# Optimization experiments

Measured on AMD Instinct MI355X. Metric: run time of the kernel, lower is better.

## Reference

```python
import jax, jax.numpy as jnp
import numpy as np

B, S, D, H = 2, 2048, 64, 12  # batch, seq, richness (per-head dim), heads
NEG = -99999.0


def setup_inputs() -> dict:
    key = jax.random.key(0)
    ks = jax.random.split(key, 9)
    s_in = 1.0 / np.sqrt(D)
    s_out = 1.0 / np.sqrt(H * D)
    return {
        "x": jax.random.normal(ks[0], (B, S, D), dtype=jnp.float32),
        "Wq": jax.random.uniform(ks[1], (D, H * D), jnp.float32, -s_in, s_in),
        "bq": jax.random.uniform(ks[2], (H * D,), jnp.float32, -s_in, s_in),
        "Wk": jax.random.uniform(ks[3], (D, H * D), jnp.float32, -s_in, s_in),
        "bk": jax.random.uniform(ks[4], (H * D,), jnp.float32, -s_in, s_in),
        "Wv": jax.random.uniform(ks[5], (D, H * D), jnp.float32, -s_in, s_in),
        "bv": jax.random.uniform(ks[6], (H * D,), jnp.float32, -s_in, s_in),
        "Wo": jax.random.uniform(ks[7], (H * D, D), jnp.float32, -s_out, s_out),
        "bo": jax.random.uniform(ks[8], (D,), jnp.float32, -s_out, s_out),
    }


def reference(x, Wq, bq, Wk, bk, Wv, bv, Wo, bo):
    b, s, d = x.shape
    def split_heads(y):
        return y.reshape(b, s, H, d).transpose(0, 2, 1, 3)  # [B,H,S,D]
    q = split_heads(x @ Wq + bq)
    k = split_heads(x @ Wk + bk)
    v = split_heads(x @ Wv + bv)
    # NOTE: no 1/sqrt(d) scaling, faithful to original module.
    scores = jnp.einsum("bhqd,bhkd->bhqk", q, k)  # [B,H,S,S]
    # Faithful quirky mask: tril of the scores, then mask where it's zero.
    mask = jnp.tril(scores)
    scores = jnp.where(mask == 0, NEG, scores)
    p = jax.nn.softmax(scores, axis=-1)
    o = jnp.einsum("bhqk,bhkd->bhqd", p, v)  # [B,H,S,D]
    o = o.transpose(0, 2, 1, 3).reshape(b, s, H * d)
    return o @ Wo + bo
```

## Files before the change

### kernel.cpp

```cpp
#include <hip/hip_runtime.h>
#include <math.h>
#include <type_traits>

#define BB 2
#define SS 2048
#define DD 64
#define HH 12
#define C2FIX 23.083120654223414f

typedef _Float16 v8h __attribute__((ext_vector_type(8)));
typedef short    v8s __attribute__((ext_vector_type(8)));
typedef short    v4s __attribute__((ext_vector_type(4)));
typedef float    v4f __attribute__((ext_vector_type(4)));
typedef unsigned int v2u __attribute__((ext_vector_type(2)));

__device__ __forceinline__ unsigned short f2bf(float f) {
    unsigned u = __float_as_uint(f);
    u += 0x7FFF + ((u >> 16) & 1);
    return (unsigned short)(u >> 16);
}

__device__ __forceinline__ void async16(const void* g, void* l) {
    __builtin_amdgcn_global_load_lds(
        (const __attribute__((address_space(1))) unsigned int*)g,
        (__attribute__((address_space(3))) unsigned int*)l, 16, 0, 0);
}

__global__ __launch_bounds__(256) void prep_kernel(
    const float* __restrict__ x,
    const float* __restrict__ Wq, const float* __restrict__ Wk,
    const float* __restrict__ Wv, const float* __restrict__ Wo,
    _Float16* __restrict__ x16, _Float16* __restrict__ W16,
    _Float16* __restrict__ WoT)
{
    const int idx = blockIdx.x * 256 + threadIdx.x;
    if (idx < 262144) {
        x16[idx] = (_Float16)x[idx];
    } else if (idx < 262144 + 147456) {
        const int t = idx - 262144;
        const int k = t / 2304, c = t % 2304;
        const int mat = c / 768, cc = c % 768;
        const float* W = (mat == 0) ? Wq : (mat == 1) ? Wk : Wv;
        W16[c * 64 + k] = (_Float16)W[k * 768 + cc];
    } else {
        const int e = idx - 262144 - 147456;
        WoT[(e & 63) * 768 + (e >> 6)] = (_Float16)Wo[e];
    }
}

__global__ __launch_bounds__(256) void qkv_kernel(
    const _Float16* __restrict__ x16, const _Float16* __restrict__ W16,
    const float* __restrict__ bq, const float* __restrict__ bk,
    const float* __restrict__ bv,
    _Float16* __restrict__ Q16, _Float16* __restrict__ K16,
    unsigned short* __restrict__ VT)
{
    const int r0  = blockIdx.x * 64;
    const int c0g = blockIdx.y * 64;
    const int mat = c0g / 768, cc0 = c0g % 768;
    const int h   = cc0 >> 6;
    const int b   = r0 >> 11, s0 = r0 & 2047;

    const int wave = threadIdx.x >> 6, lane = threadIdx.x & 63;
    const int llow = lane & 15, quad = lane >> 4;
    const int rowbase = r0 + 16 * wave;

    const float* bias = (mat == 0) ? bq : (mat == 1) ? bk : bv;

    v8h a0 = *(const v8h*)(x16 + (size_t)(rowbase + llow) * 64 + quad * 8);
    v8h a1 = *(const v8h*)(x16 + (size_t)(rowbase + llow) * 64 + 32 + quad * 8);

    v4f acc[4];
    float bv4[4];
#pragma unroll
    for (int nb = 0; nb < 4; nb++) {
        const int col = c0g + 16 * nb + llow;
        v8h b0 = *(const v8h*)(W16 + (size_t)col * 64 + quad * 8);
        v8h b1 = *(const v8h*)(W16 + (size_t)col * 64 + 32 + quad * 8);
        v4f a = (v4f){0.f, 0.f, 0.f, 0.f};
        a = __builtin_amdgcn_mfma_f32_16x16x32_f16(a0, b0, a, 0, 0, 0);
        a = __builtin_amdgcn_mfma_f32_16x16x32_f16(a1, b1, a, 0, 0, 0);
        acc[nb] = a;
        bv4[nb] = bias[cc0 + 16 * nb + llow];
    }

    const int bh = b * HH + h;
    if (mat == 0) {
#pragma unroll
        for (int nb = 0; nb < 4; nb++)
#pragma unroll
            for (int r = 0; r < 4; r++) {
                const int s = s0 + 16 * wave + quad * 4 + r;
                Q16[((size_t)bh * SS + s) * 64 + 16 * nb + llow] =
                    (_Float16)((acc[nb][r] + bv4[nb]) * 1.4426950408889634f);
            }
    } else if (mat == 1) {
#pragma unroll
        for (int nb = 0; nb < 4; nb++)
#pragma unroll
            for (int r = 0; r < 4; r++) {
                const int s = s0 + 16 * wave + quad * 4 + r;
                K16[((size_t)bh * SS + s) * 64 + 16 * nb + llow] =
                    (_Float16)(acc[nb][r] + bv4[nb]);
            }
    } else {
#pragma unroll
        for (int nb = 0; nb < 4; nb++) {
            const int d = 16 * nb + llow;
            const int s = s0 + 16 * wave + quad * 4;
            unsigned short p0 = f2bf(acc[nb][0] + bv4[nb]);
            unsigned short p1 = f2bf(acc[nb][1] + bv4[nb]);
            unsigned short p2 = f2bf(acc[nb][2] + bv4[nb]);
            unsigned short p3 = f2bf(acc[nb][3] + bv4[nb]);
            v2u pk = (v2u){(unsigned)p0 | ((unsigned)p1 << 16),
                           (unsigned)p2 | ((unsigned)p3 << 16)};
            *(v2u*)&VT[((size_t)bh * 64 + d) * SS + s] = pk;
        }
    }
}

__global__ __launch_bounds__(256, 3) void attn_kernel(
    const _Float16* __restrict__ Q16, const _Float16* __restrict__ K16,
    const unsigned short* __restrict__ VTg, _Float16* __restrict__ O16)
{
    __shared__ __align__(16) _Float16       Kl[3][64 * 64];
    __shared__ __align__(16) unsigned short Vl[3][64 * 64];

    const int bh    = blockIdx.y;
    const int qtile = (int)((blockIdx.x + 11 * blockIdx.y) & 31);
    const int qBase = qtile * 64;
    const int wave  = threadIdx.x >> 6;
    const int lane  = threadIdx.x & 63;
    const int llow  = lane & 15;
    const int quad  = lane >> 4;
    const int q0    = qBase + 16 * wave;

    const _Float16*       Kp = K16 + (size_t)bh * SS * 64;
    const unsigned short* Vp = VTg + (size_t)bh * 64 * SS;

    const _Float16* Qp = Q16 + ((size_t)bh * SS + q0) * 64;
    v8h qa0 = *(const v8h*)(Qp + llow * 64 + quad * 8);
    v8h qa1 = *(const v8h*)(Qp + llow * 64 + 32 + quad * 8);

    v4f o[4];
    v4f ls = (v4f){0.f, 0.f, 0.f, 0.f};
    const short one_bf = (short)0x3F80;
    const v4s vones = (v4s){one_bf, one_bf, one_bf, one_bf};
#pragma unroll
    for (int nb = 0; nb < 4; nb++) o[nb] = (v4f){0.f, 0.f, 0.f, 0.f};

    const int nt = qtile + 1;
    const int qrow = q0 + llow;
    const int sw = llow & 7;

    auto stage = [&](int kt, int b) {
#pragma unroll
        for (int rep = 0; rep < 2; rep++) {
            int c = rep * 256 + threadIdx.x;
            int row = c >> 3, g = (c & 7) ^ (row & 7);
            async16(Kp + (size_t)(kt + row) * 64 + g * 8,
                    &Kl[b][(rep * 256 + wave * 64) * 8]);
            async16(Vp + (size_t)row * SS + kt + g * 8,
                    &Vl[b][(rep * 256 + wave * 64) * 8]);
        }
    };

    stage(0, 0);
    if (nt > 1) stage(64, 1);

    auto round_body = [&](int t, auto masked_c) {
        constexpr bool MASKED = decltype(masked_c)::value;
        if constexpr (MASKED)
            asm volatile("s_waitcnt vmcnt(0)" ::: "memory");
        else
            asm volatile("s_waitcnt vmcnt(4)" ::: "memory");
        __builtin_amdgcn_s_barrier();
        __builtin_amdgcn_sched_barrier(0);
        if (t + 2 < nt) stage((t + 2) * 64, (t + 2) % 3);
        const int buf = t % 3, kt = t * 64;

        v4f sc[4];
#pragma unroll
        for (int cb = 0; cb < 4; cb++) {
            const int rk = 16 * cb + llow;
            v8h k0 = *(const v8h*)&Kl[buf][rk * 64 + ((quad ^ sw)) * 8];
            v8h k1 = *(const v8h*)&Kl[buf][rk * 64 + (((4 + quad) ^ sw)) * 8];
            v4f a2 = (v4f){0.f, 0.f, 0.f, 0.f};
            a2 = __builtin_amdgcn_mfma_f32_16x16x32_f16(k0, qa0, a2, 0, 0, 0);
            a2 = __builtin_amdgcn_mfma_f32_16x16x32_f16(k1, qa1, a2, 0, 0, 0);
            sc[cb] = a2;
        }

        v4s vvf[4][4];
#pragma unroll
        for (int nb = 0; nb < 4; nb++) {
            const int rv = 16 * nb + llow;
#pragma unroll
            for (int cb = 0; cb < 4; cb++)
                vvf[nb][cb] = *(const v4s*)&Vl[buf][rv * 64 +
                                (((2 * cb + (quad >> 1)) ^ sw) * 8) + (quad & 1) * 4];
        }

        v4s pA[4];
#pragma unroll
        for (int cb = 0; cb < 4; cb++) {
            const int kbase = kt + 16 * cb + quad * 4;
            unsigned dw[2];
#pragma unroll
            for (int h2 = 0; h2 < 2; h2++) {
                float pv2[2];
#pragma unroll
                for (int j2 = 0; j2 < 2; j2++) {
                    const int r = h2 * 2 + j2;
                    const float sv = sc[cb][r];
                    const float e  = __builtin_amdgcn_exp2f(sv - C2FIX);
                    float p;
                    if constexpr (MASKED)
                        p = (kbase + r <= qrow && sv != 0.f) ? e : 0.f;
                    else
                        p = (sv != 0.f) ? e : 0.f;
                    pv2[j2] = p;
                }
                dw[h2] = __builtin_amdgcn_perm(__float_as_uint(pv2[1]),
                                               __float_as_uint(pv2[0]),
                                               0x07060302u);
            }
            v2u pk = (v2u){dw[0], dw[1]};
            pA[cb] = *(const v4s*)&pk;
        }

#pragma unroll
        for (int cb = 0; cb < 4; cb++)
            ls = __builtin_amdgcn_mfma_f32_16x16x16bf16_1k(pA[cb], vones, ls, 0, 0, 0);

#pragma unroll
        for (int nb = 0; nb < 4; nb++)
#pragma unroll
            for (int cb = 0; cb < 4; cb++)
                o[nb] = __builtin_amdgcn_mfma_f32_16x16x16bf16_1k(
                            pA[cb], vvf[nb][cb], o[nb], 0, 0, 0);
    };

    for (int t = 0; t < nt - 1; t++) round_body(t, std::false_type{});
    round_body(nt - 1, std::true_type{});

    float ir[4];
#pragma unroll
    for (int r = 0; r < 4; r++)
        ir[r] = 1.0f / ls[r];
    _Float16* Op = O16 + ((size_t)bh * SS + q0) * 64;
#pragma unroll
    for (int nb = 0; nb < 4; nb++)
#pragma unroll
        for (int r = 0; r < 4; r++)
            Op[(quad * 4 + r) * 64 + 16 * nb + llow] = (_Float16)(o[nb][r] * ir[r]);
}

__global__ __launch_bounds__(256) void out_kernel(
    const _Float16* __restrict__ O16, const _Float16* __restrict__ WoT,
    const float* __restrict__ bo, float* __restrict__ out)
{
    __shared__ __align__(16) float red[4][16][66];
    const int r0   = blockIdx.x * 16;
    const int wave = threadIdx.x >> 6, lane = threadIdx.x & 63;
    const int llow = lane & 15, quad = lane >> 4;
    const int b = r0 >> 11, s = r0 & 2047;

    v4f acc[4];
#pragma unroll
    for (int cb = 0; cb < 4; cb++) acc[cb] = (v4f){0.f, 0.f, 0.f, 0.f};

#pragma unroll
    for (int i = 0; i < 6; i++) {
        const int kb = wave * 6 + i;
        const int h = kb >> 1, dseg = (kb & 1) * 32;
        v8h af = *(const v8h*)(O16 + ((size_t)(b * HH + h) * SS + s + llow) * 64 + dseg + quad * 8);
#pragma unroll
        for (int cb = 0; cb < 4; cb++) {
            v8h bf = *(const v8h*)(WoT + (size_t)(16 * cb + llow) * 768 + kb * 32 + quad * 8);
            acc[cb] = __builtin_amdgcn_mfma_f32_16x16x32_f16(af, bf, acc[cb], 0, 0, 0);
        }
    }

#pragma unroll
    for (int cb = 0; cb < 4; cb++)
#pragma unroll
        for (int r = 0; r < 4; r++)
            red[wave][quad * 4 + r][16 * cb + llow] = acc[cb][r];
    __syncthreads();

    const int col = threadIdx.x & 63, rr = threadIdx.x >> 6;
    const float bias = bo[col];
    for (int i = rr; i < 16; i += 4) {
        float sum = red[0][i][col] + red[1][i][col] + red[2][i][col] + red[3][i][col] + bias;
        out[(size_t)(r0 + i) * 64 + col] = sum;
    }
}

extern "C" void kernel_launch(void* const* d_in, const int* in_sizes, int n_in,
                              void* d_out, int out_size, void* d_ws, size_t ws_size,
                              hipStream_t stream)
{
    const float* x  = (const float*)d_in[0];
    const float* Wq = (const float*)d_in[1];
    const float* bq = (const float*)d_in[2];
    const float* Wk = (const float*)d_in[3];
    const float* bk = (const float*)d_in[4];
    const float* Wv = (const float*)d_in[5];
    const float* bv = (const float*)d_in[6];
    const float* Wo = (const float*)d_in[7];
    const float* bo = (const float*)d_in[8];
    float* out = (float*)d_out;

    char* w = (char*)d_ws;
    const size_t MB = 1024 * 1024;
    _Float16*       x16 = (_Float16*)(w);
    _Float16*       W16 = (_Float16*)(w + 512 * 1024);
    _Float16*       WoT = (_Float16*)(w + 832 * 1024);
    _Float16*       Q16 = (_Float16*)(w + 1 * MB);
    _Float16*       K16 = (_Float16*)(w + 7 * MB);
    unsigned short* VT  = (unsigned short*)(w + 13 * MB);
    _Float16*       O16 = (_Float16*)(w + 19 * MB);

    prep_kernel<<<1792, 256, 0, stream>>>(x, Wq, Wk, Wv, Wo, x16, W16, WoT);
    qkv_kernel<<<dim3(64, 36), 256, 0, stream>>>(x16, W16, bq, bk, bv, Q16, K16, VT);
    attn_kernel<<<dim3(32, BB * HH), 256, 0, stream>>>(Q16, K16, VT, O16);
    out_kernel<<<(BB * SS) / 16, 256, 0, stream>>>(O16, WoT, bo, out);
}
```

Measured before the change: 133.4 us.

## Load K/V fragments directly to registers with double buffering, drop LDS staging

Replaces the LDS triple-buffered async staging of K and V tiles in the attention kernel with direct global-to-register fragment loads, double-buffered in two register sets. The V^T layout written by the prep kernel is retiled into contiguous 64x64 blocks per key tile so each fragment load is a contiguous read. This removes LDS traffic and block barriers but raises register pressure (occupancy hint lowered from 3 to 2) and makes each wave fetch K/V from global/L2 independently, with no sharing across the 4 waves.

```diff
diff --git a/kernel.cpp b/kernel.cpp
--- a/kernel.cpp
+++ b/kernel.cpp
@@ -18,12 +18,6 @@
     unsigned u = __float_as_uint(f);
     u += 0x7FFF + ((u >> 16) & 1);
     return (unsigned short)(u >> 16);
-}
-
-__device__ __forceinline__ void async16(const void* g, void* l) {
-    __builtin_amdgcn_global_load_lds(
-        (const __attribute__((address_space(1))) unsigned int*)g,
-        (__attribute__((address_space(3))) unsigned int*)l, 16, 0, 0);
 }
 
 __global__ __launch_bounds__(256) void prep_kernel(
@@ -104,39 +98,41 @@
                     (_Float16)(acc[nb][r] + bv4[nb]);
             }
     } else {
+        const int tile = s0 >> 6;
+        const int kin  = 16 * wave + quad * 4;
 #pragma unroll
         for (int nb = 0; nb < 4; nb++) {
             const int d = 16 * nb + llow;
-            const int s = s0 + 16 * wave + quad * 4;
             unsigned short p0 = f2bf(acc[nb][0] + bv4[nb]);
             unsigned short p1 = f2bf(acc[nb][1] + bv4[nb]);
             unsigned short p2 = f2bf(acc[nb][2] + bv4[nb]);
             unsigned short p3 = f2bf(acc[nb][3] + bv4[nb]);
             v2u pk = (v2u){(unsigned)p0 | ((unsigned)p1 << 16),
                            (unsigned)p2 | ((unsigned)p3 << 16)};
-            *(v2u*)&VT[((size_t)bh * 64 + d) * SS + s] = pk;
-        }
-    }
-}
-
-__global__ __launch_bounds__(256, 3) void attn_kernel(
+            *(v2u*)&VT[(((size_t)bh * 32 + tile) * 64 + d) * 64 + kin] = pk;
+        }
+    }
+}
+
+struct Frags {
+    v8h k[8];
+    v4s v[16];
+};
+
+__global__ __launch_bounds__(256, 2) void attn_kernel(
     const _Float16* __restrict__ Q16, const _Float16* __restrict__ K16,
     const unsigned short* __restrict__ VTg, _Float16* __restrict__ O16)
 {
-    __shared__ __align__(16) _Float16       Kl[3][64 * 64];
-    __shared__ __align__(16) unsigned short Vl[3][64 * 64];
-
     const int bh    = blockIdx.y;
     const int qtile = (int)((blockIdx.x + 11 * blockIdx.y) & 31);
-    const int qBase = qtile * 64;
     const int wave  = threadIdx.x >> 6;
     const int lane  = threadIdx.x & 63;
     const int llow  = lane & 15;
     const int quad  = lane >> 4;
-    const int q0    = qBase + 16 * wave;
-
-    const _Float16*       Kp = K16 + (size_t)bh * SS * 64;
-    const unsigned short* Vp = VTg + (size_t)bh * 64 * SS;
+    const int q0    = qtile * 64 + 16 * wave;
+
+    const _Float16*       Kp  = K16 + (size_t)bh * SS * 64;
+    const unsigned short* Vp2 = VTg + (size_t)bh * 32 * 4096;
 
     const _Float16* Qp = Q16 + ((size_t)bh * SS + q0) * 64;
     v8h qa0 = *(const v8h*)(Qp + llow * 64 + quad * 8);
@@ -149,56 +145,38 @@
 #pragma unroll
     for (int nb = 0; nb < 4; nb++) o[nb] = (v4f){0.f, 0.f, 0.f, 0.f};
 
-    const int nt = qtile + 1;
+    const int nt   = qtile + 1;
     const int qrow = q0 + llow;
-    const int sw = llow & 7;
-
-    auto stage = [&](int kt, int b) {
-#pragma unroll
-        for (int rep = 0; rep < 2; rep++) {
-            int c = rep * 256 + threadIdx.x;
-            int row = c >> 3, g = (c & 7) ^ (row & 7);
-            async16(Kp + (size_t)(kt + row) * 64 + g * 8,
-                    &Kl[b][(rep * 256 + wave * 64) * 8]);
-            async16(Vp + (size_t)row * SS + kt + g * 8,
-                    &Vl[b][(rep * 256 + wave * 64) * 8]);
-        }
+
+    Frags fA, fB;
+
+    auto stageT = [&](Frags& f, int t) {
+        const _Float16* kb = Kp + (size_t)t * 64 * 64;
+#pragma unroll
+        for (int cb = 0; cb < 4; cb++) {
+            f.k[cb * 2 + 0] = *(const v8h*)(kb + (16 * cb + llow) * 64 + quad * 8);
+            f.k[cb * 2 + 1] = *(const v8h*)(kb + (16 * cb + llow) * 64 + 32 + quad * 8);
+        }
+        const unsigned short* vb = Vp2 + (size_t)t * 4096;
+#pragma unroll
+        for (int nb = 0; nb < 4; nb++)
+#pragma unroll
+            for (int cb = 0; cb < 4; cb++)
+                f.v[nb * 4 + cb] = *(const v4s*)(vb + (16 * nb + llow) * 64
+                                                 + 16 * cb + 4 * quad);
     };
 
-    stage(0, 0);
-    if (nt > 1) stage(64, 1);
-
-    auto round_body = [&](int t, auto masked_c) {
+    auto computeT = [&](int t, Frags& f, auto masked_c) {
         constexpr bool MASKED = decltype(masked_c)::value;
-        if constexpr (MASKED)
-            asm volatile("s_waitcnt vmcnt(0)" ::: "memory");
-        else
-            asm volatile("s_waitcnt vmcnt(4)" ::: "memory");
-        __builtin_amdgcn_s_barrier();
-        __builtin_amdgcn_sched_barrier(0);
-        if (t + 2 < nt) stage((t + 2) * 64, (t + 2) % 3);
-        const int buf = t % 3, kt = t * 64;
+        const int kt = t * 64;
 
         v4f sc[4];
 #pragma unroll
         for (int cb = 0; cb < 4; cb++) {
-            const int rk = 16 * cb + llow;
-            v8h k0 = *(const v8h*)&Kl[buf][rk * 64 + ((quad ^ sw)) * 8];
-            v8h k1 = *(const v8h*)&Kl[buf][rk * 64 + (((4 + quad) ^ sw)) * 8];
             v4f a2 = (v4f){0.f, 0.f, 0.f, 0.f};
-            a2 = __builtin_amdgcn_mfma_f32_16x16x32_f16(k0, qa0, a2, 0, 0, 0);
-            a2 = __builtin_amdgcn_mfma_f32_16x16x32_f16(k1, qa1, a2, 0, 0, 0);
+            a2 = __builtin_amdgcn_mfma_f32_16x16x32_f16(f.k[cb * 2 + 0], qa0, a2, 0, 0, 0);
+            a2 = __builtin_amdgcn_mfma_f32_16x16x32_f16(f.k[cb * 2 + 1], qa1, a2, 0, 0, 0);
             sc[cb] = a2;
-        }
-
-        v4s vvf[4][4];
-#pragma unroll
-        for (int nb = 0; nb < 4; nb++) {
-            const int rv = 16 * nb + llow;
-#pragma unroll
-            for (int cb = 0; cb < 4; cb++)
-                vvf[nb][cb] = *(const v4s*)&Vl[buf][rv * 64 +
-                                (((2 * cb + (quad >> 1)) ^ sw) * 8) + (quad & 1) * 4];
         }
 
         v4s pA[4];
@@ -238,11 +216,23 @@
 #pragma unroll
             for (int cb = 0; cb < 4; cb++)
                 o[nb] = __builtin_amdgcn_mfma_f32_16x16x16bf16_1k(
-                            pA[cb], vvf[nb][cb], o[nb], 0, 0, 0);
+                            pA[cb], f.v[nb * 4 + cb], o[nb], 0, 0, 0);
     };
 
-    for (int t = 0; t < nt - 1; t++) round_body(t, std::false_type{});
-    round_body(nt - 1, std::true_type{});
+    stageT(fA, 0);
+    int t = 0;
+    while (t + 2 <= nt - 1) {
+        stageT(fB, t + 1); computeT(t, fA, std::false_type{});
+        stageT(fA, t + 2); computeT(t + 1, fB, std::false_type{});
+        t += 2;
+    }
+    if (t == nt - 2) {
+        stageT(fB, t + 1);
+        computeT(t, fA, std::false_type{});
+        computeT(t + 1, fB, std::true_type{});
+    } else {
+        computeT(t, fA, std::true_type{});
+    }
 
     float ir[4];
 #pragma unroll
```

New measurement: 286.4 us. +114.6%, slower.
